# Kernel optimization log

Hardware: AMD Instinct MI355X
Metric: run time of the kernel (lower is better)

Reference implementation:

```python
import jax, jax.numpy as jnp
import numpy as np

N = 512       # building thermal nodes (state dim)
M = 9         # inputs: [Tout(t), Q_1..Q_8]
T = 20000     # RK4 grid points
DT = 30.0     # seconds per step (as in docstring example)
N_DATA = 2000 # outside-temperature breakpoints for interp


def setup_inputs() -> dict:
    key = jax.random.key(0)
    kA, kB, kQ, kT, kiv = jax.random.split(key, 5)
    # Stable continuous-time system: spectral radius ~5e-3 -> |lambda*dt| ~ 0.2
    A = (jax.random.normal(kA, (N, N), jnp.float32) * 1e-4
         - 5e-3 * jnp.eye(N, dtype=jnp.float32))
    B = jax.random.normal(kB, (N, M), jnp.float32) * 1e-3
    Q = jax.random.uniform(kQ, (M - 1,), jnp.float32) * 100.0  # heat gains
    t_eval = jnp.arange(T, dtype=jnp.float32) * DT
    # interp1d replacement: sorted breakpoints + diurnal temperature signal
    Tout_t = jnp.linspace(0.0, T * DT, N_DATA).astype(jnp.float32)
    Tout_v = (15.0 + 10.0 * jnp.sin(2.0 * jnp.pi * Tout_t / 86400.0)
              + jax.random.normal(kT, (N_DATA,), jnp.float32))
    iv = 20.0 + jax.random.normal(kiv, (N,), jnp.float32)
    return {"A": A, "B": B, "Q": Q, "Tout_t": Tout_t, "Tout_v": Tout_v,
            "iv": iv, "t_eval": t_eval}


def reference(A, B, Q, Tout_t, Tout_v, iv, t_eval):
    """RK4 (torchdiffeq 3/8-rule fixed-grid) integration of dx/dt = A@x + B@u(t)."""

    def f(t, x):
        Tout = jnp.interp(t, Tout_t, Tout_v)          # on-device interp1d
        u = jnp.concatenate([Tout[None], Q])          # [M]
        return A @ x + B @ u                          # [N]

    def step(x, td):
        t, dt = td
        k1 = f(t, x)
        k2 = f(t + dt / 3.0, x + dt * k1 / 3.0)
        k3 = f(t + dt * 2.0 / 3.0, x + dt * (k2 - k1 / 3.0))
        k4 = f(t + dt, x + dt * (k1 - k2 + k3))
        x_new = x + dt * (k1 + 3.0 * (k2 + k3) + k4) / 8.0
        return x_new, x_new

    ts = t_eval[:-1]
    dts = jnp.diff(t_eval)
    _, xs = jax.lax.scan(step, iv, (ts, dts))         # [T-1, N]
    return jnp.concatenate([iv[None, :], xs], axis=0)  # [T, N]
```

## Files before the change

### kernel.cpp

```cpp
#include <hip/hip_runtime.h>

#define TT    20000
#define CCH   2500
#define RROWS 2501
#define NDATA 2000
#define MSZ   262144

static constexpr size_t OFF_HT  = 0;
static constexpr size_t OFF_H2T = (size_t)MSZ;
static constexpr size_t OFF_MP  = 2*(size_t)MSZ;
static constexpr size_t OFF_SQ  = 10*(size_t)MSZ;
static constexpr size_t OFF_VEC = 12*(size_t)MSZ;
static constexpr size_t OFF_FJ  = OFF_VEC + 4096;
static constexpr size_t OFF_AL  = OFF_FJ + 163840;
static constexpr size_t OFF_SA  = OFF_AL + 102400;
static constexpr size_t OFF_SB  = OFF_SA + (size_t)RROWS*512;

#define MICRO_FMA(a, b) do { \
  acc0.x += (a).x*(b).x; acc0.y += (a).x*(b).y; acc0.z += (a).x*(b).z; acc0.w += (a).x*(b).w; \
  acc1.x += (a).y*(b).x; acc1.y += (a).y*(b).y; acc1.z += (a).y*(b).z; acc1.w += (a).y*(b).w; \
  acc2.x += (a).z*(b).x; acc2.y += (a).z*(b).y; acc2.z += (a).z*(b).z; acc2.w += (a).z*(b).w; \
  acc3.x += (a).w*(b).x; acc3.y += (a).w*(b).y; acc3.z += (a).w*(b).z; acc3.w += (a).w*(b).w; \
} while (0)

#define DECL_GEMM_VARS() \
    int t = threadIdx.x; \
    int tx = t & 15, ty = t >> 4; \
    int ar = t & 63, ak4 = (t >> 6) * 4; \
    int bk = t >> 4, bc4 = (t & 15) * 4; \
    float4 acc0 = {0,0,0,0}, acc1 = {0,0,0,0}, acc2 = {0,0,0,0}, acc3 = {0,0,0,0}; \
    (void)tx; (void)ty; (void)ar; (void)ak4; (void)bk; (void)bc4

#define GEMM_CORE_DB(LOADA, LOADB) \
    { float4 ra = LOADA(0); float4 rbv = LOADB(0); \
    As[0][ak4+0][ar]=ra.x; As[0][ak4+1][ar]=ra.y; As[0][ak4+2][ar]=ra.z; As[0][ak4+3][ar]=ra.w; \
    *(float4*)&Bs[0][bk][bc4] = rbv; \
    for (int kt = 1; kt <= 32; kt++) { \
        __syncthreads(); \
        const int cur = (kt - 1) & 1; \
        if (kt < 32) { ra = LOADA(kt); rbv = LOADB(kt); } \
        _Pragma("unroll") \
        for (int kk = 0; kk < 16; kk++) { \
            float4 a = *(const float4*)&As[cur][kk][ty*4]; \
            float4 b = *(const float4*)&Bs[cur][kk][tx*4]; \
            MICRO_FMA(a, b); \
        } \
        if (kt < 32) { const int nb = kt & 1; \
            As[nb][ak4+0][ar]=ra.x; As[nb][ak4+1][ar]=ra.y; As[nb][ak4+2][ar]=ra.z; As[nb][ak4+3][ar]=ra.w; \
            *(float4*)&Bs[nb][bk][bc4] = rbv; } \
    } }

__device__ __forceinline__ void pow_tile(const float* __restrict__ Ap,
                                         const float* __restrict__ Bp,
                                         float* __restrict__ Zp, int idx) {
    __shared__ float As[2][16][68], Bs[2][16][68];
    DECL_GEMM_VARS();
    int rb = (idx >> 3) * 64, cb = (idx & 7) * 64;
#define LA(kt) (*(const float4*)&Ap[(size_t)(rb+ar)*512 + (kt)*16 + ak4])
#define LB(kt) (*(const float4*)&Bp[(size_t)((kt)*16+bk)*512 + cb + bc4])
    GEMM_CORE_DB(LA, LB)
#undef LA
#undef LB
    size_t zb = (size_t)(rb + ty*4)*512 + cb + tx*4;
    *(float4*)&Zp[zb]        = acc0;
    *(float4*)&Zp[zb + 512]  = acc1;
    *(float4*)&Zp[zb + 1024] = acc2;
    *(float4*)&Zp[zb + 1536] = acc3;
}

__device__ __forceinline__ void matvecT128(const float* __restrict__ MT,
                                           const float* __restrict__ x,
                                           float* __restrict__ y, int rb,
                                           const float* __restrict__ gc,
                                           const float* __restrict__ gu1,
                                           const float* __restrict__ gu2) {
    __shared__ float xs[512];
    __shared__ float red2[2][128];
    int t = threadIdx.x;
    xs[t] = x[t]; xs[t + 256] = x[t + 256];
    __syncthreads();
    int rl = t & 127, h = t >> 7;
    size_t col = (size_t)rb + rl;
    float acc = 0.f;
    int k0 = h << 8;
    #pragma unroll 4
    for (int k = k0; k < k0 + 256; k++) acc += MT[(size_t)k*512 + col] * xs[k];
    red2[h][rl] = acc;
    __syncthreads();
    if (t < 128) {
        float s = red2[0][t] + red2[1][t];
        int r = rb + t;
        if (gc) y[r] = 30.f * (gc[r] + 0.5f*gu1[r] + (1.f/6.f)*gu2[r] + (1.f/24.f)*s);
        else    y[r] = s;
    }
}

__device__ __forceinline__ float interp1(float tt, const float* __restrict__ xp,
                                         const float* __restrict__ fp) {
    if (tt <= xp[0]) return fp[0];
    if (tt >= xp[NDATA-1]) return fp[NDATA-1];
    int lo = 0, hi = NDATA - 1;
    while (hi - lo > 1) { int mid = (lo + hi) >> 1; if (xp[mid] <= tt) lo = mid; else hi = mid; }
    float x0 = xp[lo], x1 = xp[lo+1];
    return fp[lo] + (fp[lo+1] - fp[lo]) * (tt - x0) / (x1 - x0);
}

__global__ __launch_bounds__(256) void k_setup(const float* __restrict__ A,
        const float* __restrict__ B, const float* __restrict__ Q,
        const float* __restrict__ te, const float* __restrict__ Tt,
        const float* __restrict__ Tv, const float* __restrict__ iv,
        float* __restrict__ HT, float* __restrict__ vec, float* __restrict__ AL,
        float* __restrict__ out, float* __restrict__ SA) {
    int bx = blockIdx.x, t = threadIdx.x;
    if (bx < 256) {
        __shared__ float Ts[32][33];
        int tr = bx >> 4, tc = bx & 15;
        int rl = t >> 3, cl4 = (t & 7) * 4;
        float4 a = *(const float4*)&A[(size_t)(tr*32 + rl)*512 + tc*32 + cl4];
        Ts[rl][cl4+0] = 30.f*a.x; Ts[rl][cl4+1] = 30.f*a.y;
        Ts[rl][cl4+2] = 30.f*a.z; Ts[rl][cl4+3] = 30.f*a.w;
        __syncthreads();
        float4 o;
        o.x = Ts[cl4+0][rl]; o.y = Ts[cl4+1][rl]; o.z = Ts[cl4+2][rl]; o.w = Ts[cl4+3][rl];
        *(float4*)&HT[(size_t)(tc*32 + rl)*512 + tr*32 + cl4] = o;
    } else if (bx == 256) {
        for (int i = t; i < 512; i += 256) {
            float v = B[i*9];
            float c = 0.f;
            #pragma unroll
            for (int j = 0; j < 8; j++) c += B[i*9 + 1 + j] * Q[j];
            vec[i] = v;
            vec[2560 + i] = c;
        }
    } else if (bx == 257) {
        for (int i = t; i < 512; i += 256) { out[i] = iv[i]; SA[i] = iv[i]; }
    } else {
        int n = (bx - 258) * 256 + t;
        if (n >= TT) return;
        float* a = AL + (size_t)n * 5;
        if (n == TT - 1) { a[0]=a[1]=a[2]=a[3]=a[4]=0.f; return; }
        float tt = te[n];
        float T1 = interp1(tt, Tt, Tv);
        float T2 = interp1(tt + 10.f, Tt, Tv);
        float T3 = interp1(tt + 20.f, Tt, Tv);
        float T4 = interp1(tt + 30.f, Tt, Tv);
        a[0] = 3.75f * (T1 + 3.f*T2 + 3.f*T3 + T4);
        a[1] = 3.75f * (T1 + 2.f*T2 + T3);
        a[2] = 3.75f * (T1*(1.f/3.f) + T2);
        a[3] = 1.25f * T1;
        a[4] = 1.f;
    }
}

__global__ __launch_bounds__(256) void k_h2kv(const float* __restrict__ HT,
                                              float* __restrict__ H2T,
                                              float* __restrict__ vec) {
    int bx = blockIdx.x;
    if (bx < 64) { pow_tile(HT, HT, H2T, bx); return; }
    int sub = bx - 64, which = sub >> 2, rb = (sub & 3) * 128;
    if (which == 0) matvecT128(HT, vec,        vec + 512,  rb, 0, 0, 0);
    else            matvecT128(HT, vec + 2560, vec + 3072, rb, 0, 0, 0);
}

__global__ __launch_bounds__(256) void k_m1kv(const float* __restrict__ HT,
                                              const float* __restrict__ H2T,
                                              float* __restrict__ M1T,
                                              float* __restrict__ vec) {
    int bx = blockIdx.x;
    if (bx < 64) {
        __shared__ float As[2][16][68], Bs[2][16][68];
        DECL_GEMM_VARS();
        int rb = (bx >> 3) * 64, cb = (bx & 7) * 64;
#define LA(kt) ({ size_t off = (size_t)(rb+ar)*512 + (kt)*16 + ak4; \
        float4 h  = *(const float4*)&HT[off]; \
        float4 h2 = *(const float4*)&H2T[off]; \
        float4 r_; \
        r_.x = h.x*(1.f/6.f) + h2.x*(1.f/24.f); r_.y = h.y*(1.f/6.f) + h2.y*(1.f/24.f); \
        r_.z = h.z*(1.f/6.f) + h2.z*(1.f/24.f); r_.w = h.w*(1.f/6.f) + h2.w*(1.f/24.f); \
        int dd = (rb+ar) - ((kt)*16 + ak4); \
        if (dd >= 0 && dd < 4) (&r_.x)[dd] += 0.5f; \
        r_; })
#define LB(kt) (*(const float4*)&H2T[(size_t)((kt)*16+bk)*512 + cb + bc4])
        GEMM_CORE_DB(LA, LB)
#undef LA
#undef LB
        int col = cb + tx*4;
        #pragma unroll
        for (int i = 0; i < 4; i++) {
            int r = rb + ty*4 + i;
            float4 h = *(const float4*)&HT[(size_t)r*512 + col];
            float4* ac = (i==0) ? &acc0 : (i==1) ? &acc1 : (i==2) ? &acc2 : &acc3;
            ac->x += h.x + (r == col+0 ? 1.f : 0.f);
            ac->y += h.y + (r == col+1 ? 1.f : 0.f);
            ac->z += h.z + (r == col+2 ? 1.f : 0.f);
            ac->w += h.w + (r == col+3 ? 1.f : 0.f);
            *(float4*)&M1T[(size_t)r*512 + col] = *ac;
        }
        return;
    }
    int sub = bx - 64, which = sub >> 2, rb = (sub & 3) * 128;
    if (which == 0) matvecT128(HT, vec + 512,  vec + 1024, rb, 0, 0, 0);
    else            matvecT128(HT, vec + 3072, vec + 3584, rb, 0, 0, 0);
}

__global__ __launch_bounds__(256) void k_m2kv(const float* __restrict__ M1T,
                                              float* __restrict__ M2T,
                                              const float* __restrict__ HT,
                                              float* __restrict__ vec) {
    int bx = blockIdx.x;
    if (bx < 64) { pow_tile(M1T, M1T, M2T, bx); return; }
    int sub = bx - 64, which = sub >> 2, rb = (sub & 3) * 128;
    if (which == 0) matvecT128(HT, vec + 1024, vec + 1536, rb, 0, 0, 0);
    else matvecT128(HT, vec + 3584, vec + 2048, rb,
                    vec + 2560, vec + 3072, vec + 3584);
}

__global__ __launch_bounds__(256) void k_pow(const float* __restrict__ A,
                                             const float* __restrict__ B0,
                                             float* __restrict__ Z0) {
    int sel = blockIdx.x >> 6;
    pow_tile(A, B0 + (size_t)sel*MSZ, Z0 + (size_t)sel*MSZ, blockIdx.x & 63);
}

__global__ __launch_bounds__(256) void k_wgen_sq(const float* __restrict__ vec,
                                                 const float* __restrict__ MP,
                                                 float* __restrict__ FJ,
                                                 const float* __restrict__ P,
                                                 float* __restrict__ Pout) {
    int bx = blockIdx.x;
    if (bx >= 64) { pow_tile(P, P, Pout, bx - 64); return; }
    int d = bx >> 3, cb = (bx & 7) * 64;
    int t = threadIdx.x;
    if (d == 0) {
        for (int idx = t; idx < 320; idx += 256) {
            int r = idx >> 6, c = idx & 63;
            float s = vec[(size_t)r*512 + cb + c];
            #pragma unroll
            for (int i = 0; i < 8; i++)
                FJ[((size_t)i*40 + i*5 + r)*512 + cb + c] = s;
        }
        for (int j = 0; j < 7; j++)
            for (int i = j + 1; i < 8; i++)
                for (int idx = t; idx < 320; idx += 256) {
                    int r = idx >> 6, c = idx & 63;
                    FJ[((size_t)j*40 + i*5 + r)*512 + cb + c] = 0.f;
                }
        return;
    }
    __shared__ float Ws[5][512];
    __shared__ float red4[4][5][64];
    const float* Mj = MP + (size_t)(d - 1)*MSZ;
    for (int e = t; e < 2560; e += 256) Ws[e >> 9][e & 511] = vec[e];
    __syncthreads();
    int col = t & 63, kq = t >> 6, k0 = kq * 128;
    float acc[5] = {0.f, 0.f, 0.f, 0.f, 0.f};
    #pragma unroll 4
    for (int k = k0; k < k0 + 128; k++) {
        float m = Mj[(size_t)k*512 + cb + col];
        acc[0] += Ws[0][k]*m; acc[1] += Ws[1][k]*m; acc[2] += Ws[2][k]*m;
        acc[3] += Ws[3][k]*m; acc[4] += Ws[4][k]*m;
    }
    #pragma unroll
    for (int r = 0; r < 5; r++) red4[kq][r][col] = acc[r];
    __syncthreads();
    for (int idx = t; idx < 320; idx += 256) {
        int r = idx >> 6, c = idx & 63;
        float s = red4[0][r][c] + red4[1][r][c] + red4[2][r][c] + red4[3][r][c];
        for (int i = 0; i + d < 8; i++)
            FJ[((size_t)(i + d)*40 + i*5 + r)*512 + cb + c] = s;
    }
}

__global__ __launch_bounds__(256) void k_e40_sq(const float* __restrict__ AL,
                                                const float* __restrict__ FJ,
                                                float* __restrict__ SA1,
                                                const float* __restrict__ P,
                                                float* __restrict__ Pout) {
    int bx = blockIdx.x;
    if (bx >= 320) { pow_tile(P, P, Pout, bx - 320); return; }
    const float* GT = FJ + (size_t)7*40*512;
    int kb = (bx >> 3) * 64, cb = (bx & 7) * 64;
    __shared__ float Ah[64][41], Bsv[40][68];
    int t = threadIdx.x;
    int tx = t & 15, ty = t >> 4;
    #pragma unroll
    for (int m = 0; m < 10; m++) {
        int e = t + 256*m;
        int row = e / 40, q = e - 40*row;
        float v = 0.f;
        if (kb + row < CCH) v = AL[(size_t)(kb + row)*40 + q];
        Ah[row][q] = v;
        int fq = e >> 6, fc = e & 63;
        Bsv[fq][fc] = GT[(size_t)fq*512 + cb + fc];
    }
    __syncthreads();
    float4 acc0 = {0,0,0,0}, acc1 = {0,0,0,0}, acc2 = {0,0,0,0}, acc3 = {0,0,0,0};
    #pragma unroll 8
    for (int q = 0; q < 40; q++) {
        float4 b = *(const float4*)&Bsv[q][tx*4];
        float a0 = Ah[ty*4+0][q], a1 = Ah[ty*4+1][q];
        float a2 = Ah[ty*4+2][q], a3 = Ah[ty*4+3][q];
        acc0.x += a0*b.x; acc0.y += a0*b.y; acc0.z += a0*b.z; acc0.w += a0*b.w;
        acc1.x += a1*b.x; acc1.y += a1*b.y; acc1.z += a1*b.z; acc1.w += a1*b.w;
        acc2.x += a2*b.x; acc2.y += a2*b.y; acc2.z += a2*b.z; acc2.w += a2*b.w;
        acc3.x += a3*b.x; acc3.y += a3*b.y; acc3.z += a3*b.z; acc3.w += a3*b.w;
    }
    int col = cb + tx*4;
    #pragma unroll
    for (int i = 0; i < 4; i++) {
        int k = kb + ty*4 + i;
        if (k < CCH) {
            float4 a = (i==0) ? acc0 : (i==1) ? acc1 : (i==2) ? acc2 : acc3;
            *(float4*)&SA1[(size_t)k*512 + col] = a;
        }
    }
}

__global__ __launch_bounds__(256) void k_scan_sq(const float* __restrict__ Ain,
                                                 float* __restrict__ Aout,
                                                 const float* __restrict__ QT, int shift,
                                                 const float* __restrict__ P,
                                                 float* __restrict__ Pout) {
    int bx = blockIdx.x;
    if (bx >= 320) { pow_tile(P, P, Pout, bx - 320); return; }
    __shared__ float As[2][16][68], Bs[2][16][68];
    DECL_GEMM_VARS();
    int kb = (bx >> 3) * 64, cb = (bx & 7) * 64;
    int xr = kb + ar - shift;
    bool aval = (xr >= 0) && (kb + ar < RROWS);
#define LA(kt) ({ float4 z = {0,0,0,0}; \
        if (aval) z = *(const float4*)&Ain[(size_t)xr*512 + (kt)*16 + ak4]; z; })
#define LB(kt) (*(const float4*)&QT[(size_t)((kt)*16+bk)*512 + cb + bc4])
    GEMM_CORE_DB(LA, LB)
#undef LA
#undef LB
    int col = cb + tx*4;
    #pragma unroll
    for (int i = 0; i < 4; i++) {
        int krow = kb + ty*4 + i;
        if (krow < RROWS) {
            float4 own = *(const float4*)&Ain[(size_t)krow*512 + col];
            float4 a = (i==0) ? acc0 : (i==1) ? acc1 : (i==2) ? acc2 : acc3;
            float4 res = {own.x + a.x, own.y + a.y, own.z + a.z, own.w + a.w};
            *(float4*)&Aout[(size_t)krow*512 + col] = res;
        }
    }
}

__global__ __launch_bounds__(256) void k_final(const float* __restrict__ SS,
                                               const float* __restrict__ MP,
                                               const float* __restrict__ AL,
                                               const float* __restrict__ FJ,
                                               float* __restrict__ out) {
    __shared__ float smem[8096];
    float (*As)[132] = (float(*)[132])smem;
    float (*Bs)[68]  = (float(*)[68])(smem + 2112);
    int t = threadIdx.x;
    int tx = t & 15, ty = t >> 4;
    int ar = t & 127, ak8 = (t >> 7) * 8;
    int bk = t >> 4, bc4 = (t & 15) * 4;
    int j = blockIdx.x >> 3;
    const float* Bm = MP + (size_t)j*MSZ;
    int cb = (blockIdx.x & 7) * 64;
    int kb = blockIdx.y * 128;
    bool aval = (kb + ar < CCH);
    float4 acc[8];
    #pragma unroll
    for (int r = 0; r < 8; r++) acc[r] = (float4){0.f, 0.f, 0.f, 0.f};
    for (int kt = 0; kt < 32; kt++) {
        float4 a0 = {0,0,0,0}, a1 = {0,0,0,0};
        if (aval) {
            a0 = *(const float4*)&SS[(size_t)(kb+ar)*512 + kt*16 + ak8];
            a1 = *(const float4*)&SS[(size_t)(kb+ar)*512 + kt*16 + ak8 + 4];
        }
        float4 bv = *(const float4*)&Bm[(size_t)(kt*16+bk)*512 + cb + bc4];
        As[ak8+0][ar]=a0.x; As[ak8+1][ar]=a0.y; As[ak8+2][ar]=a0.z; As[ak8+3][ar]=a0.w;
        As[ak8+4][ar]=a1.x; As[ak8+5][ar]=a1.y; As[ak8+6][ar]=a1.z; As[ak8+7][ar]=a1.w;
        *(float4*)&Bs[bk][bc4] = bv;
        __syncthreads();
        #pragma unroll
        for (int kk = 0; kk < 16; kk++) {
            float4 aA = *(const float4*)&As[kk][ty*8];
            float4 aB = *(const float4*)&As[kk][ty*8 + 4];
            float4 b  = *(const float4*)&Bs[kk][tx*4];
            acc[0].x += aA.x*b.x; acc[0].y += aA.x*b.y; acc[0].z += aA.x*b.z; acc[0].w += aA.x*b.w;
            acc[1].x += aA.y*b.x; acc[1].y += aA.y*b.y; acc[1].z += aA.y*b.z; acc[1].w += aA.y*b.w;
            acc[2].x += aA.z*b.x; acc[2].y += aA.z*b.y; acc[2].z += aA.z*b.z; acc[2].w += aA.z*b.w;
            acc[3].x += aA.w*b.x; acc[3].y += aA.w*b.y; acc[3].z += aA.w*b.z; acc[3].w += aA.w*b.w;
            acc[4].x += aB.x*b.x; acc[4].y += aB.x*b.y; acc[4].z += aB.x*b.z; acc[4].w += aB.x*b.w;
            acc[5].x += aB.y*b.x; acc[5].y += aB.y*b.y; acc[5].z += aB.y*b.z; acc[5].w += aB.y*b.w;
            acc[6].x += aB.z*b.x; acc[6].y += aB.z*b.y; acc[6].z += aB.z*b.z; acc[6].w += aB.z*b.w;
            acc[7].x += aB.w*b.x; acc[7].y += aB.w*b.y; acc[7].z += aB.w*b.z; acc[7].w += aB.w*b.w;
        }
        __syncthreads();
    }
    float (*Ah)[42] = (float(*)[42])smem;
    float (*Fs)[68] = (float(*)[68])(smem + 5376);
    #pragma unroll
    for (int m = 0; m < 20; m++) {
        int e = t + 256*m;
        int row = e / 40, q = e - 40*row;
        float v = 0.f;
        if (kb + row < CCH) v = AL[(size_t)(kb + row)*40 + q];
        Ah[row][q] = v;
    }
    #pragma unroll
    for (int m = 0; m < 10; m++) {
        int e = t + 256*m;
        int fq = e >> 6, fc = e & 63;
        Fs[fq][fc] = FJ[(size_t)j*40*512 + (size_t)fq*512 + cb + fc];
    }
    __syncthreads();
    #pragma unroll 8
    for (int q = 0; q < 40; q++) {
        float4 b = *(const float4*)&Fs[q][tx*4];
        #pragma unroll
        for (int r = 0; r < 8; r++) {
            float a = Ah[ty*8 + r][q];
            acc[r].x += a*b.x; acc[r].y += a*b.y; acc[r].z += a*b.z; acc[r].w += a*b.w;
        }
    }
    int col = cb + tx*4;
    #pragma unroll
    for (int r = 0; r < 8; r++) {
        int k = kb + ty*8 + r;
        int n = 8*k + j + 1;
        if (k < CCH && n < TT)
            *(float4*)&out[(size_t)n*512 + col] = acc[r];
    }
}

extern "C" void kernel_launch(void* const* d_in, const int* in_sizes, int n_in,
                              void* d_out, int out_size, void* d_ws, size_t ws_size,
                              hipStream_t stream) {
    const float* A  = (const float*)d_in[0];
    const float* B  = (const float*)d_in[1];
    const float* Q  = (const float*)d_in[2];
    const float* Tt = (const float*)d_in[3];
    const float* Tv = (const float*)d_in[4];
    const float* iv = (const float*)d_in[5];
    const float* te = (const float*)d_in[6];
    float* out = (float*)d_out;
    float* w = (float*)d_ws;

    float* HT  = w + OFF_HT;
    float* H2T = w + OFF_H2T;
    float* MP  = w + OFF_MP;
    float* SQ  = w + OFF_SQ;
    float* vec = w + OFF_VEC;
    float* FJ  = w + OFF_FJ;
    float* AL  = w + OFF_AL;
    float* SA  = w + OFF_SA;
    float* SB  = w + OFF_SB;

    float* M16 = H2T;
    float* M32 = HT;
    float* M64 = SQ;
    float* M8  = MP + 7*(size_t)MSZ;

    k_setup<<<337, 256, 0, stream>>>(A, B, Q, te, Tt, Tv, iv, HT, vec, AL, out, SA);
    k_h2kv<<<72, 256, 0, stream>>>(HT, H2T, vec);
    k_m1kv<<<72, 256, 0, stream>>>(HT, H2T, MP, vec);
    k_m2kv<<<72, 256, 0, stream>>>(MP, MP + MSZ, HT, vec);
    k_pow<<<128, 256, 0, stream>>>(MP + MSZ, MP, MP + 2*(size_t)MSZ);
    k_pow<<<256, 256, 0, stream>>>(MP + 3*(size_t)MSZ, MP, MP + 4*(size_t)MSZ);
    k_wgen_sq<<<128, 256, 0, stream>>>(vec, MP, FJ, M8, M16);
    k_e40_sq<<<384, 256, 0, stream>>>(AL, FJ, SA + 512, M16, M32);
    k_scan_sq<<<384, 256, 0, stream>>>(SA, SB, M8,  1, M32, M64);
    k_scan_sq<<<320, 256, 0, stream>>>(SB, SA, M16, 2, nullptr, nullptr);
    k_scan_sq<<<320, 256, 0, stream>>>(SA, SB, M32, 4, nullptr, nullptr);
    k_scan_sq<<<320, 256, 0, stream>>>(SB, SA, M64, 8, nullptr, nullptr);
    k_final<<<dim3(64, 20), 256, 0, stream>>>(SA, MP, AL, FJ, out);
}
```

Measured before the change: 526.4 us.

## Use bf16 MFMA for final state-expansion GEMM with pre-transposed bf16 matrices

Adds a prep kernel that converts the eight propagation matrices to bf16 and transposes them. The final GEMM kernel now converts the scanned states to bf16 on the fly and runs 16x16x32 bf16 MFMA instead of fp32 FMA. This is meant to cut the compute cost of the largest output-producing GEMM. It gives up accuracy, since the state and propagator are rounded to bf16, and it adds an extra conversion kernel launch.

```diff
diff --git a/kernel.cpp b/kernel.cpp
--- a/kernel.cpp
+++ b/kernel.cpp
@@ -5,6 +5,11 @@
 #define RROWS 2501
 #define NDATA 2000
 #define MSZ   262144
+
+typedef unsigned short u16;
+typedef unsigned int   u32;
+using f32x4 = __attribute__((ext_vector_type(4))) float;
+using s16x8 = __attribute__((ext_vector_type(8))) short;
 
 static constexpr size_t OFF_HT  = 0;
 static constexpr size_t OFF_H2T = (size_t)MSZ;
@@ -15,6 +20,12 @@
 static constexpr size_t OFF_AL  = OFF_FJ + 163840;
 static constexpr size_t OFF_SA  = OFF_AL + 102400;
 static constexpr size_t OFF_SB  = OFF_SA + (size_t)RROWS*512;
+
+__device__ __forceinline__ u16 f2bf(float f) {
+    u32 u = __float_as_uint(f);
+    u += 0x7fff + ((u >> 16) & 1);
+    return (u16)(u >> 16);
+}
 
 #define MICRO_FMA(a, b) do { \
   acc0.x += (a).x*(b).x; acc0.y += (a).x*(b).y; acc0.z += (a).x*(b).z; acc0.w += (a).x*(b).w; \
@@ -347,86 +358,135 @@
     }
 }
 
+__global__ __launch_bounds__(256) void k_mprep(const float* __restrict__ MPin,
+                                               u16* __restrict__ Mbf) {
+    int j = blockIdx.x >> 6, tile = blockIdx.x & 63;
+    int kb = (tile >> 3) * 64, cb = (tile & 7) * 64;
+    const float* MT = MPin + (size_t)j * MSZ;
+    __shared__ float Ts[64][65];
+    int t = threadIdx.x;
+    int lr = t >> 4, lc = (t & 15) * 4;
+    #pragma unroll
+    for (int p = 0; p < 4; p++) {
+        float4 v = *(const float4*)&MT[(size_t)(kb + p*16 + lr)*512 + cb + lc];
+        Ts[p*16+lr][lc+0] = v.x; Ts[p*16+lr][lc+1] = v.y;
+        Ts[p*16+lr][lc+2] = v.z; Ts[p*16+lr][lc+3] = v.w;
+    }
+    __syncthreads();
+    int r = t >> 2, c16 = (t & 3) * 16;
+    u32 pk[8];
+    #pragma unroll
+    for (int i = 0; i < 8; i++) {
+        u32 a = f2bf(Ts[c16 + 2*i][r]);
+        u32 b = f2bf(Ts[c16 + 2*i + 1][r]);
+        pk[i] = a | (b << 16);
+    }
+    u16* dst = Mbf + (size_t)j*MSZ + (size_t)(cb + r)*512 + kb + c16;
+    *(uint4*)dst       = make_uint4(pk[0], pk[1], pk[2], pk[3]);
+    *(uint4*)(dst + 8) = make_uint4(pk[4], pk[5], pk[6], pk[7]);
+}
+
 __global__ __launch_bounds__(256) void k_final(const float* __restrict__ SS,
-                                               const float* __restrict__ MP,
+                                               const u16* __restrict__ Mbf,
                                                const float* __restrict__ AL,
                                                const float* __restrict__ FJ,
                                                float* __restrict__ out) {
-    __shared__ float smem[8096];
-    float (*As)[132] = (float(*)[132])smem;
-    float (*Bs)[68]  = (float(*)[68])(smem + 2112);
+    __shared__ float smem[8448];
+    u16* Asu = (u16*)smem;
+    u16* Bsu = (u16*)(smem + 2560);
     int t = threadIdx.x;
-    int tx = t & 15, ty = t >> 4;
-    int ar = t & 127, ak8 = (t >> 7) * 8;
-    int bk = t >> 4, bc4 = (t & 15) * 4;
+    int lane = t & 63, w = t >> 6;
+    int lo16 = lane & 15, hi = lane >> 4;
     int j = blockIdx.x >> 3;
-    const float* Bm = MP + (size_t)j*MSZ;
     int cb = (blockIdx.x & 7) * 64;
     int kb = blockIdx.y * 128;
-    bool aval = (kb + ar < CCH);
-    float4 acc[8];
-    #pragma unroll
-    for (int r = 0; r < 8; r++) acc[r] = (float4){0.f, 0.f, 0.f, 0.f};
-    for (int kt = 0; kt < 32; kt++) {
-        float4 a0 = {0,0,0,0}, a1 = {0,0,0,0};
-        if (aval) {
-            a0 = *(const float4*)&SS[(size_t)(kb+ar)*512 + kt*16 + ak8];
-            a1 = *(const float4*)&SS[(size_t)(kb+ar)*512 + kt*16 + ak8 + 4];
-        }
-        float4 bv = *(const float4*)&Bm[(size_t)(kt*16+bk)*512 + cb + bc4];
-        As[ak8+0][ar]=a0.x; As[ak8+1][ar]=a0.y; As[ak8+2][ar]=a0.z; As[ak8+3][ar]=a0.w;
-        As[ak8+4][ar]=a1.x; As[ak8+5][ar]=a1.y; As[ak8+6][ar]=a1.z; As[ak8+7][ar]=a1.w;
-        *(float4*)&Bs[bk][bc4] = bv;
+    const u16* Bm = Mbf + (size_t)j * MSZ;
+
+    f32x4 acc[2][4];
+    #pragma unroll
+    for (int m = 0; m < 2; m++)
+        #pragma unroll
+        for (int n = 0; n < 4; n++) acc[m][n] = 0.f;
+
+    int s_row = t >> 3;
+    int s_k4  = (t & 7) * 4;
+    int b_row = t >> 2;
+    int b_k8  = (t & 3) * 8;
+
+    for (int kt = 0; kt < 16; kt++) {
         __syncthreads();
         #pragma unroll
-        for (int kk = 0; kk < 16; kk++) {
-            float4 aA = *(const float4*)&As[kk][ty*8];
-            float4 aB = *(const float4*)&As[kk][ty*8 + 4];
-            float4 b  = *(const float4*)&Bs[kk][tx*4];
-            acc[0].x += aA.x*b.x; acc[0].y += aA.x*b.y; acc[0].z += aA.x*b.z; acc[0].w += aA.x*b.w;
-            acc[1].x += aA.y*b.x; acc[1].y += aA.y*b.y; acc[1].z += aA.y*b.z; acc[1].w += aA.y*b.w;
-            acc[2].x += aA.z*b.x; acc[2].y += aA.z*b.y; acc[2].z += aA.z*b.z; acc[2].w += aA.z*b.w;
-            acc[3].x += aA.w*b.x; acc[3].y += aA.w*b.y; acc[3].z += aA.w*b.z; acc[3].w += aA.w*b.w;
-            acc[4].x += aB.x*b.x; acc[4].y += aB.x*b.y; acc[4].z += aB.x*b.z; acc[4].w += aB.x*b.w;
-            acc[5].x += aB.y*b.x; acc[5].y += aB.y*b.y; acc[5].z += aB.y*b.z; acc[5].w += aB.y*b.w;
-            acc[6].x += aB.z*b.x; acc[6].y += aB.z*b.y; acc[6].z += aB.z*b.z; acc[6].w += aB.z*b.w;
-            acc[7].x += aB.w*b.x; acc[7].y += aB.w*b.y; acc[7].z += aB.w*b.z; acc[7].w += aB.w*b.w;
+        for (int p = 0; p < 4; p++) {
+            int r = p*32 + s_row;
+            float4 v = {0.f, 0.f, 0.f, 0.f};
+            if (kb + r < CCH) v = *(const float4*)&SS[(size_t)(kb+r)*512 + kt*32 + s_k4];
+            uint2 pk;
+            pk.x = (u32)f2bf(v.x) | ((u32)f2bf(v.y) << 16);
+            pk.y = (u32)f2bf(v.z) | ((u32)f2bf(v.w) << 16);
+            *(uint2*)&Asu[r*40 + s_k4] = pk;
+        }
+        {
+            uint4 v = *(const uint4*)&Bm[(size_t)(cb + b_row)*512 + kt*32 + b_k8];
+            *(uint4*)&Bsu[b_row*40 + b_k8] = v;
         }
         __syncthreads();
-    }
-    float (*Ah)[42] = (float(*)[42])smem;
-    float (*Fs)[68] = (float(*)[68])(smem + 5376);
-    #pragma unroll
-    for (int m = 0; m < 20; m++) {
-        int e = t + 256*m;
-        int row = e / 40, q = e - 40*row;
-        float v = 0.f;
-        if (kb + row < CCH) v = AL[(size_t)(kb + row)*40 + q];
-        Ah[row][q] = v;
-    }
-    #pragma unroll
-    for (int m = 0; m < 10; m++) {
-        int e = t + 256*m;
-        int fq = e >> 6, fc = e & 63;
-        Fs[fq][fc] = FJ[(size_t)j*40*512 + (size_t)fq*512 + cb + fc];
-    }
-    __syncthreads();
-    #pragma unroll 8
-    for (int q = 0; q < 40; q++) {
-        float4 b = *(const float4*)&Fs[q][tx*4];
-        #pragma unroll
-        for (int r = 0; r < 8; r++) {
-            float a = Ah[ty*8 + r][q];
-            acc[r].x += a*b.x; acc[r].y += a*b.y; acc[r].z += a*b.z; acc[r].w += a*b.w;
-        }
-    }
-    int col = cb + tx*4;
-    #pragma unroll
-    for (int r = 0; r < 8; r++) {
-        int k = kb + ty*8 + r;
-        int n = 8*k + j + 1;
-        if (k < CCH && n < TT)
-            *(float4*)&out[(size_t)n*512 + col] = acc[r];
+        s16x8 a0 = *(const s16x8*)&Asu[(w*32      + lo16)*40 + hi*8];
+        s16x8 a1 = *(const s16x8*)&Asu[(w*32 + 16 + lo16)*40 + hi*8];
+        #pragma unroll
+        for (int n = 0; n < 4; n++) {
+            s16x8 b = *(const s16x8*)&Bsu[(n*16 + lo16)*40 + hi*8];
+            acc[0][n] = __builtin_amdgcn_mfma_f32_16x16x32_bf16(a0, b, acc[0][n], 0, 0, 0);
+            acc[1][n] = __builtin_amdgcn_mfma_f32_16x16x32_bf16(a1, b, acc[1][n], 0, 0, 0);
+        }
+    }
+    __syncthreads();
+    float (*Ah)[44] = (float(*)[44])smem;
+    float (*Fs)[44] = (float(*)[44])(smem + 5632);
+    {
+        int row = t >> 1, half = t & 1;
+        #pragma unroll
+        for (int i = 0; i < 5; i++) {
+            float4 v = {0.f, 0.f, 0.f, 0.f};
+            if (kb + row < CCH) v = *(const float4*)&AL[(size_t)(kb+row)*40 + half*20 + i*4];
+            *(float4*)&Ah[row][half*20 + i*4] = v;
+        }
+        #pragma unroll
+        for (int m = 0; m < 10; m++) {
+            int e = t + 256*m;
+            int q = e >> 6, c = e & 63;
+            Fs[c][q] = FJ[(size_t)j*40*512 + (size_t)q*512 + cb + c];
+        }
+    }
+    __syncthreads();
+    #pragma unroll
+    for (int cq = 0; cq < 10; cq++) {
+        float4 bv[4];
+        #pragma unroll
+        for (int n = 0; n < 4; n++) bv[n] = *(const float4*)&Fs[n*16 + lo16][cq*4];
+        #pragma unroll
+        for (int m = 0; m < 2; m++) {
+            #pragma unroll
+            for (int r = 0; r < 4; r++) {
+                float4 av = *(const float4*)&Ah[w*32 + m*16 + hi*4 + r][cq*4];
+                #pragma unroll
+                for (int n = 0; n < 4; n++) {
+                    acc[m][n][r] += av.x*bv[n].x + av.y*bv[n].y + av.z*bv[n].z + av.w*bv[n].w;
+                }
+            }
+        }
+    }
+    #pragma unroll
+    for (int m = 0; m < 2; m++) {
+        #pragma unroll
+        for (int r = 0; r < 4; r++) {
+            int k = kb + w*32 + m*16 + hi*4 + r;
+            int n_out = 8*k + j + 1;
+            if (k < CCH && n_out < TT) {
+                #pragma unroll
+                for (int n = 0; n < 4; n++)
+                    out[(size_t)n_out*512 + cb + n*16 + lo16] = acc[m][n][r];
+            }
+        }
     }
 }
 
@@ -457,6 +517,7 @@
     float* M32 = HT;
     float* M64 = SQ;
     float* M8  = MP + 7*(size_t)MSZ;
+    u16*   Mbf = (u16*)SB;
 
     k_setup<<<337, 256, 0, stream>>>(A, B, Q, te, Tt, Tv, iv, HT, vec, AL, out, SA);
     k_h2kv<<<72, 256, 0, stream>>>(HT, H2T, vec);
@@ -470,5 +531,6 @@
     k_scan_sq<<<320, 256, 0, stream>>>(SB, SA, M16, 2, nullptr, nullptr);
     k_scan_sq<<<320, 256, 0, stream>>>(SA, SB, M32, 4, nullptr, nullptr);
     k_scan_sq<<<320, 256, 0, stream>>>(SB, SA, M64, 8, nullptr, nullptr);
-    k_final<<<dim3(64, 20), 256, 0, stream>>>(SA, MP, AL, FJ, out);
-}
+    k_mprep<<<512, 256, 0, stream>>>(MP, Mbf);
+    k_final<<<dim3(64, 20), 256, 0, stream>>>(SA, Mbf, AL, FJ, out);
+}
```

New measurement: 553.4 us. 1.05x slower.
